# Kernel optimization log

Hardware: AMD Instinct MI355X
Metric: run time of the kernel (lower is better)

Reference implementation:

```python
import jax, jax.numpy as jnp
import numpy as np

L, V, C, H, T_MAX, FF = 8, 50257, 1024, 16, 1024, 4096
DH = C // H
EPS = 1e-5


def setup_inputs() -> dict:
    key = jax.random.key(0)
    ks = jax.random.split(key, 16)
    s = 0.02
    inp = {
        "idx": jax.random.randint(ks[0], (2, 1024), 0, V, dtype=jnp.int32),
        "tok_emb": jax.random.normal(ks[1], (V, C), jnp.float32) * s,
        "pos_emb": jax.random.normal(ks[2], (T_MAX, C), jnp.float32) * s,
        "qkv_w": jax.random.normal(ks[3], (L, C, 3 * C), jnp.float32) * s,
        "qkv_b": jnp.zeros((L, 3 * C), jnp.float32),
        "out_w": jax.random.normal(ks[4], (L, C, C), jnp.float32) * s,
        "out_b": jnp.zeros((L, C), jnp.float32),
        "ln1_s": jnp.ones((L, C), jnp.float32),
        "ln1_b": jnp.zeros((L, C), jnp.float32),
        "ln2_s": jnp.ones((L, C), jnp.float32),
        "ln2_b": jnp.zeros((L, C), jnp.float32),
        "ffn_w1": jax.random.normal(ks[5], (L, C, FF), jnp.float32) * s,
        "ffn_b1": jnp.zeros((L, FF), jnp.float32),
        "ffn_w2": jax.random.normal(ks[6], (L, FF, C), jnp.float32) * s,
        "ffn_b2": jnp.zeros((L, C), jnp.float32),
        "lnf_s": jnp.ones((C,), jnp.float32),
        "lnf_b": jnp.zeros((C,), jnp.float32),
    }
    return inp


def _layernorm(x, scale, bias):
    m = jnp.mean(x, axis=-1, keepdims=True)
    v = jnp.mean(jnp.square(x - m), axis=-1, keepdims=True)
    return (x - m) * jax.lax.rsqrt(v + EPS) * scale + bias


def reference(idx, tok_emb, pos_emb, qkv_w, qkv_b, out_w, out_b,
              ln1_s, ln1_b, ln2_s, ln2_b,
              ffn_w1, ffn_b1, ffn_w2, ffn_b2, lnf_s, lnf_b):
    B, T = idx.shape
    x = tok_emb[idx] + pos_emb[:T]          # [B,T,C]
    causal = jnp.tril(jnp.ones((T, T), bool))  # [T,T]
    scale = 1.0 / np.sqrt(DH)

    def block(x, p):
        qw, qb, ow, ob, l1s, l1b, l2s, l2b, w1, b1, w2, b2 = p
        h = _layernorm(x, l1s, l1b)
        qkv = h @ qw + qb                    # [B,T,3C]
        q, k, v = jnp.split(qkv, 3, axis=-1)
        q = q.reshape(B, T, H, DH).transpose(0, 2, 1, 3)  # [B,H,T,Dh]
        k = k.reshape(B, T, H, DH).transpose(0, 2, 1, 3)
        v = v.reshape(B, T, H, DH).transpose(0, 2, 1, 3)
        scores = jnp.einsum('bhqd,bhkd->bhqk', q, k) * scale
        scores = jnp.where(causal, scores, -jnp.inf)
        w = jax.nn.softmax(scores, axis=-1)
        o = jnp.einsum('bhqk,bhkd->bhqd', w, v)
        o = o.transpose(0, 2, 1, 3).reshape(B, T, C)
        x = x + (o @ ow + ob)
        h2 = _layernorm(x, l2s, l2b)
        x = x + (jax.nn.gelu(h2 @ w1 + b1, approximate=False) @ w2 + b2)
        return x, None

    params = (qkv_w, qkv_b, out_w, out_b, ln1_s, ln1_b, ln2_s, ln2_b,
              ffn_w1, ffn_b1, ffn_w2, ffn_b2)
    x, _ = jax.lax.scan(block, x, params)
    x = _layernorm(x, lnf_s, lnf_b)
    logits = x @ tok_emb.T                   # tied head, no bias
    return logits
```

## Files before the change

### kernel.cpp

```cpp
#include <hip/hip_runtime.h>
#include <hip/hip_bf16.h>

#define NL 8
#define NV 50257
#define NC 1024
#define NH 16
#define NT 1024
#define NFF 4096
#define NB 2
#define NM (NB*NT)

typedef __attribute__((ext_vector_type(8))) short bf16x8;
typedef __attribute__((ext_vector_type(4))) float f32x4;

__device__ __forceinline__ unsigned short f2bf(float f) {
    union { float f; unsigned u; } a; a.f = f;
    unsigned r = a.u + 0x7FFFu + ((a.u >> 16) & 1u);
    return (unsigned short)(r >> 16);
}

__device__ __forceinline__ void gload16(const unsigned short* g, unsigned short* l) {
    __builtin_amdgcn_global_load_lds(
        (const __attribute__((address_space(1))) unsigned int*)g,
        (__attribute__((address_space(3))) unsigned int*)l,
        16, 0, 0);
}

template<int VN> __device__ __forceinline__ void vwait() {
    asm volatile("s_waitcnt vmcnt(%0)" :: "n"(VN) : "memory");
}
__device__ __forceinline__ void barrier_mem() {
    asm volatile("" ::: "memory");
    __builtin_amdgcn_s_barrier();
    asm volatile("" ::: "memory");
}

__global__ __launch_bounds__(256) void embed_kernel(
    const int* __restrict__ idx, const float* __restrict__ te,
    const float* __restrict__ pe, float* __restrict__ x) {
    int row = blockIdx.x;
    int t = row & (NT - 1);
    int id = idx[row];
    const float4 a = reinterpret_cast<const float4*>(te + (size_t)id * NC)[threadIdx.x];
    const float4 b = reinterpret_cast<const float4*>(pe + (size_t)t * NC)[threadIdx.x];
    float4 o; o.x = a.x + b.x; o.y = a.y + b.y; o.z = a.z + b.z; o.w = a.w + b.w;
    reinterpret_cast<float4*>(x + (size_t)row * NC)[threadIdx.x] = o;
}

__global__ __launch_bounds__(256) void cvt_bf16_kernel(
    const float* __restrict__ in, unsigned short* __restrict__ out, size_t n4) {
    size_t i = (size_t)blockIdx.x * 256 + threadIdx.x;
    if (i >= n4) return;
    float4 v = reinterpret_cast<const float4*>(in)[i];
    uint2 u;
    u.x = (unsigned)f2bf(v.x) | ((unsigned)f2bf(v.y) << 16);
    u.y = (unsigned)f2bf(v.z) | ((unsigned)f2bf(v.w) << 16);
    reinterpret_cast<uint2*>(out)[i] = u;
}

__global__ __launch_bounds__(256) void wtrans4_kernel(
    const float* __restrict__ s0, const float* __restrict__ s1,
    const float* __restrict__ s2, const float* __restrict__ s3,
    unsigned short* __restrict__ d0, unsigned short* __restrict__ d1,
    unsigned short* __restrict__ d2, unsigned short* __restrict__ d3) {
    __shared__ float tile[32][33];
    int bid = blockIdx.x;
    const float* W; unsigned short* D; int K, N, tn, tk;
    if (bid < 3072)      { W = s0; D = d0; K = 1024; N = 3072; tn = bid % 96;  tk = bid / 96; }
    else if (bid < 4096) { int t = bid - 3072; W = s1; D = d1; K = 1024; N = 1024; tn = t & 31;  tk = t >> 5; }
    else if (bid < 8192) { int t = bid - 4096; W = s2; D = d2; K = 1024; N = 4096; tn = t & 127; tk = t >> 7; }
    else                 { int t = bid - 8192; W = s3; D = d3; K = 4096; N = 1024; tn = t & 31;  tk = t >> 5; }
    int n0 = tn * 32, k0 = tk * 32;
    int tx = threadIdx.x, ty = threadIdx.y;
#pragma unroll
    for (int i = 0; i < 4; ++i)
        tile[ty + i * 8][tx] = W[(size_t)(k0 + ty + i * 8) * N + n0 + tx];
    __syncthreads();
#pragma unroll
    for (int i = 0; i < 4; ++i)
        D[(size_t)(n0 + ty + i * 8) * K + k0 + tx] = f2bf(tile[tx][ty + i * 8]);
}

__global__ __launch_bounds__(256) void ln_kernel(
    const float* __restrict__ x, const float* __restrict__ gam,
    const float* __restrict__ bet, unsigned short* __restrict__ out) {
    __shared__ float red[4];
    int row = blockIdx.x, tid = threadIdx.x;
    const float4 v = reinterpret_cast<const float4*>(x + (size_t)row * NC)[tid];
    float s = v.x + v.y + v.z + v.w;
#pragma unroll
    for (int m = 32; m >= 1; m >>= 1) s += __shfl_xor(s, m, 64);
    if ((tid & 63) == 0) red[tid >> 6] = s;
    __syncthreads();
    float mean = (red[0] + red[1] + red[2] + red[3]) * (1.0f / NC);
    __syncthreads();
    float dx = v.x - mean, dy = v.y - mean, dz = v.z - mean, dw = v.w - mean;
    float q = dx * dx + dy * dy + dz * dz + dw * dw;
#pragma unroll
    for (int m = 32; m >= 1; m >>= 1) q += __shfl_xor(q, m, 64);
    if ((tid & 63) == 0) red[tid >> 6] = q;
    __syncthreads();
    float var = (red[0] + red[1] + red[2] + red[3]) * (1.0f / NC);
    float rstd = rsqrtf(var + 1e-5f);
    int c = tid * 4;
    const float4 g4 = reinterpret_cast<const float4*>(gam)[tid];
    const float4 b4 = reinterpret_cast<const float4*>(bet)[tid];
    uint2 u;
    u.x = (unsigned)f2bf(dx * rstd * g4.x + b4.x) |
          ((unsigned)f2bf(dy * rstd * g4.y + b4.y) << 16);
    u.y = (unsigned)f2bf(dz * rstd * g4.z + b4.z) |
          ((unsigned)f2bf(dw * rstd * g4.w + b4.w) << 16);
    reinterpret_cast<uint2*>(out + (size_t)row * NC + c)[0] = u;
}

template<int ACT, bool BIAS, bool OUTBF16, bool ATOMIC>
__global__ __launch_bounds__(256) void gemm_kernel(
    const unsigned short* __restrict__ A, const unsigned short* __restrict__ Bt,
    const float* __restrict__ bias, void* __restrict__ Cout,
    int N, int K, int ldc, int ksub) {
    __shared__ unsigned short As[2][128 * 32];
    __shared__ unsigned short Bs[2][128 * 32];
    const int tid = threadIdx.x;
    const int lane = tid & 63;
    const int wave = tid >> 6;
    const int wm = wave >> 1, wn = wave & 1;
    const int lr = lane & 15, lg = lane >> 4;
    const int m0 = blockIdx.x * 128, n0 = blockIdx.y * 128;
    const int kbeg = blockIdx.z * ksub, kend = kbeg + ksub;

    const int r0 = tid >> 2;
    const int c0 = (tid & 3) * 8;
    const unsigned short* Ag0 = A + (size_t)(m0 + r0) * K + c0;
    const unsigned short* Ag1 = A + (size_t)(m0 + r0 + 64) * K + c0;
    const unsigned short* Bg0 = Bt + (size_t)(n0 + r0) * K + c0;
    const unsigned short* Bg1 = Bt + (size_t)(n0 + r0 + 64) * K + c0;
    const int dw0 = wave * 512;
    const int dw1 = 2048 + wave * 512;

    const f32x4 zero4 = {0.0f, 0.0f, 0.0f, 0.0f};
    f32x4 acc[4][4];
#pragma unroll
    for (int i = 0; i < 4; ++i)
#pragma unroll
        for (int j = 0; j < 4; ++j) acc[i][j] = zero4;

    auto stage = [&](int buf, int k0) {
        gload16(Ag0 + k0, &As[buf][dw0]);
        gload16(Ag1 + k0, &As[buf][dw1]);
        gload16(Bg0 + k0, &Bs[buf][dw0]);
        gload16(Bg1 + k0, &Bs[buf][dw1]);
    };

    stage(0, kbeg);
    __syncthreads();
    int cur = 0;
    for (int k0 = kbeg; k0 < kend; k0 += 32) {
        if (k0 + 32 < kend) stage(cur ^ 1, k0 + 32);
        bf16x8 af[4], bfr[4];
#pragma unroll
        for (int f = 0; f < 4; ++f) {
            af[f]  = *reinterpret_cast<const bf16x8*>(&As[cur][(wm * 64 + f * 16 + lr) * 32 + lg * 8]);
            bfr[f] = *reinterpret_cast<const bf16x8*>(&Bs[cur][(wn * 64 + f * 16 + lr) * 32 + lg * 8]);
        }
#pragma unroll
        for (int i = 0; i < 4; ++i)
#pragma unroll
            for (int j = 0; j < 4; ++j)
                acc[i][j] = __builtin_amdgcn_mfma_f32_16x16x32_bf16(af[i], bfr[j], acc[i][j], 0, 0, 0);
        __syncthreads();
        cur ^= 1;
    }

#pragma unroll
    for (int i = 0; i < 4; ++i) {
#pragma unroll
        for (int j = 0; j < 4; ++j) {
            int col = n0 + wn * 64 + j * 16 + lr;
            float bv = (BIAS && kbeg == 0) ? bias[col] : 0.0f;
#pragma unroll
            for (int r = 0; r < 4; ++r) {
                int row = m0 + wm * 64 + i * 16 + lg * 4 + r;
                float v = acc[i][j][r] + bv;
                if (ACT == 1) v = 0.5f * v * (1.0f + erff(v * 0.70710678118654752f));
                if (ATOMIC) {
                    atomicAdd(reinterpret_cast<float*>(Cout) + (size_t)row * ldc + col, v);
                } else if (OUTBF16) {
                    reinterpret_cast<unsigned short*>(Cout)[(size_t)row * ldc + col] = f2bf(v);
                } else {
                    reinterpret_cast<float*>(Cout)[(size_t)row * ldc + col] = v;
                }
            }
        }
    }
}

__global__ __launch_bounds__(512, 2) void head_gemm_kernel(
    const unsigned short* __restrict__ A, const unsigned short* __restrict__ Bt,
    float* __restrict__ C, int N, int K) {
    __shared__ unsigned short lds[4][2][8192];
    const int tid = threadIdx.x;
    const int lane = tid & 63, wid = tid >> 6;
    const int wm = wid >> 2, wn = wid & 3;
    const int lr = lane & 15, lg = lane >> 4;

    const int qx = gridDim.x >> 3;
    const int orig = blockIdx.x;
    const int wg = (orig & 7) * qx + (orig >> 3);
    const int m0 = (wg & 7) * 256;
    const int n0 = (wg >> 3) * 256;

    const int o0 = tid, o1 = tid + 512;
    int rA0, kb0, rA1, kb1;
    { int pr = o0 >> 3, s = o0 & 7; int li = (s << 4) ^ ((pr & 7) << 4);
      rA0 = (pr << 1) | (li >> 6); kb0 = li & 63; }
    { int pr = o1 >> 3, s = o1 & 7; int li = (s << 4) ^ ((pr & 7) << 4);
      rA1 = (pr << 1) | (li >> 6); kb1 = li & 63; }
    const char* pA0 = (const char*)A + (size_t)(m0 + rA0) * (2 * K) + kb0;
    const char* pA1 = (const char*)A + (size_t)(m0 + rA1) * (2 * K) + kb1;
    const char* pB0 = (const char*)Bt + (size_t)min(n0 + rA0, N - 1) * (2 * K) + kb0;
    const char* pB1 = (const char*)Bt + (size_t)min(n0 + rA1, N - 1) * (2 * K) + kb1;
    const int dw0 = wid * 512;
    const int dw1 = 4096 + wid * 512;

    const int swz = (((lr & 1) << 6) | (lg << 4)) ^ (((lr >> 1) & 7) << 4);
    const int pbA = (wm * 64 + (lr >> 1)) * 128 + swz;
    const int pbB = (wn * 32 + (lr >> 1)) * 128 + swz;

    auto stage = [&](int slot, int koff) {
        unsigned short* la = &lds[slot][0][0];
        unsigned short* lb = &lds[slot][1][0];
        gload16((const unsigned short*)(pA0 + koff), la + dw0);
        gload16((const unsigned short*)(pA1 + koff), la + dw1);
        gload16((const unsigned short*)(pB0 + koff), lb + dw0);
        gload16((const unsigned short*)(pB1 + koff), lb + dw1);
    };
    auto rdA = [&](int slot, int mf) -> bf16x8 {
        return *reinterpret_cast<const bf16x8*>(
            (const char*)lds + slot * 32768 + pbA + mf * 1024);
    };
    auto rdB = [&](int slot, int nf) -> bf16x8 {
        return *reinterpret_cast<const bf16x8*>(
            (const char*)lds + slot * 32768 + 16384 + pbB + nf * 1024);
    };

    const f32x4 zero4 = {0.0f, 0.0f, 0.0f, 0.0f};
    f32x4 acc[8][4];
#pragma unroll
    for (int i = 0; i < 8; ++i)
#pragma unroll
        for (int j = 0; j < 4; ++j) acc[i][j] = zero4;

#define MFMA_ROW(AF, MI) \
    acc[MI][0] = __builtin_amdgcn_mfma_f32_16x16x32_bf16(AF, bf0, acc[MI][0], 0, 0, 0); \
    acc[MI][1] = __builtin_amdgcn_mfma_f32_16x16x32_bf16(AF, bf1, acc[MI][1], 0, 0, 0); \
    acc[MI][2] = __builtin_amdgcn_mfma_f32_16x16x32_bf16(AF, bf2, acc[MI][2], 0, 0, 0); \
    acc[MI][3] = __builtin_amdgcn_mfma_f32_16x16x32_bf16(AF, bf3, acc[MI][3], 0, 0, 0);

    stage(0, 0);
    stage(1, 64);
    const int nk = K >> 6;
    for (int t = 0; t < nk; ++t) {
        const int cur = (t & 1) << 1;
        const int koff = t << 7;
        const bool pf = (t + 1 < nk);
        vwait<4>();
        barrier_mem();
        if (pf) stage(cur ^ 2, koff + 128);
        bf16x8 bf0 = rdB(cur, 0), bf1 = rdB(cur, 1), bf2 = rdB(cur, 2), bf3 = rdB(cur, 3);
        bf16x8 a0 = rdA(cur, 0), a1 = rdA(cur, 1), a2 = rdA(cur, 2), a3 = rdA(cur, 3);
        __builtin_amdgcn_s_setprio(1);
        MFMA_ROW(a0, 0) MFMA_ROW(a1, 1) MFMA_ROW(a2, 2) MFMA_ROW(a3, 3)
        __builtin_amdgcn_s_setprio(0);
        if (pf) stage((cur ^ 2) | 1, koff + 192);
        a0 = rdA(cur, 4); a1 = rdA(cur, 5); a2 = rdA(cur, 6); a3 = rdA(cur, 7);
        __builtin_amdgcn_s_setprio(1);
        MFMA_ROW(a0, 4) MFMA_ROW(a1, 5) MFMA_ROW(a2, 6) MFMA_ROW(a3, 7)
        __builtin_amdgcn_s_setprio(0);
        if (pf) vwait<8>(); else vwait<0>();
        barrier_mem();
        const int nxt = cur | 1;
        bf0 = rdB(nxt, 0); bf1 = rdB(nxt, 1); bf2 = rdB(nxt, 2); bf3 = rdB(nxt, 3);
        a0 = rdA(nxt, 0); a1 = rdA(nxt, 1); a2 = rdA(nxt, 2); a3 = rdA(nxt, 3);
        __builtin_amdgcn_s_setprio(1);
        MFMA_ROW(a0, 0) MFMA_ROW(a1, 1) MFMA_ROW(a2, 2) MFMA_ROW(a3, 3)
        __builtin_amdgcn_s_setprio(0);
        a0 = rdA(nxt, 4); a1 = rdA(nxt, 5); a2 = rdA(nxt, 6); a3 = rdA(nxt, 7);
        __builtin_amdgcn_s_setprio(1);
        MFMA_ROW(a0, 4) MFMA_ROW(a1, 5) MFMA_ROW(a2, 6) MFMA_ROW(a3, 7)
        __builtin_amdgcn_s_setprio(0);
    }
#undef MFMA_ROW

#pragma unroll
    for (int mf = 0; mf < 8; ++mf)
#pragma unroll
        for (int nf = 0; nf < 4; ++nf) {
            int col = n0 + wn * 64 + nf * 16 + lr;
            if (col < N) {
#pragma unroll
                for (int r = 0; r < 4; ++r) {
                    int row = m0 + wm * 128 + mf * 16 + lg * 4 + r;
                    C[(size_t)row * N + col] = acc[mf][nf][r];
                }
            }
        }
}

__global__ __launch_bounds__(256) void vtrans_kernel(
    const unsigned short* __restrict__ qkv, unsigned short* __restrict__ vt) {
    __shared__ unsigned short tile[32][33];
    int bh = blockIdx.z; int b = bh >> 4, h = bh & 15;
    int t0 = blockIdx.x * 32, d0 = blockIdx.y * 32;
    int tx = threadIdx.x, ty = threadIdx.y;
#pragma unroll
    for (int i = 0; i < 4; ++i)
        tile[ty + i * 8][tx] =
            qkv[(size_t)(b * NT + t0 + ty + i * 8) * 3072 + 2048 + h * 64 + d0 + tx];
    __syncthreads();
#pragma unroll
    for (int i = 0; i < 4; ++i)
        vt[((size_t)(b * NH + h) * 64 + d0 + ty + i * 8) * NT + t0 + tx] = tile[tx][ty + i * 8];
}

__global__ __launch_bounds__(64) void attn_kernel(
    const unsigned short* __restrict__ qkv, const unsigned short* __restrict__ vt,
    unsigned short* __restrict__ o) {
    __shared__ unsigned short Vs[64][72];
    __shared__ unsigned short Ps[32][72];
    const int qt = blockIdx.x;
    const int h  = blockIdx.y;
    const int b  = blockIdx.z;
    const int lane = threadIdx.x;
    const int lr = lane & 15, lg = lane >> 4;

    const unsigned short* qbase = qkv + (size_t)(b * NT + qt * 32) * 3072 + h * 64;
    bf16x8 qf[2][2];
#pragma unroll
    for (int mf = 0; mf < 2; ++mf)
#pragma unroll
        for (int kc = 0; kc < 2; ++kc)
            qf[mf][kc] = *reinterpret_cast<const bf16x8*>(
                qbase + (size_t)(mf * 16 + lr) * 3072 + kc * 32 + lg * 8);

    const f32x4 zero4 = {0.0f, 0.0f, 0.0f, 0.0f};
    f32x4 oacc[2][4];
    float mrow[2][4], lsum[2][4];
#pragma unroll
    for (int mf = 0; mf < 2; ++mf) {
#pragma unroll
        for (int nf = 0; nf < 4; ++nf) oacc[mf][nf] = zero4;
#pragma unroll
        for (int r = 0; r < 4; ++r) { mrow[mf][r] = -INFINITY; lsum[mf][r] = 0.0f; }
    }

    const int qend = qt * 32 + 32;
    const int nkt = (qend + 63) >> 6;
    const unsigned short* kbase = qkv + (size_t)(b * NT) * 3072 + NC + h * 64;
    const unsigned short* vbase = vt + (size_t)((b * NH + h) * 64) * NT;

    for (int kt = 0; kt < nkt; ++kt) {
        __syncthreads();
#pragma unroll
        for (int i = 0; i < 8; ++i) {
            int chunk = lane + i * 64;
            int d = chunk >> 3;
            int kk = (chunk & 7) * 8;
            *reinterpret_cast<bf16x8*>(&Vs[d][kk]) =
                *reinterpret_cast<const bf16x8*>(vbase + (size_t)d * NT + kt * 64 + kk);
        }
        f32x4 s[2][4];
#pragma unroll
        for (int mf = 0; mf < 2; ++mf)
#pragma unroll
            for (int jf = 0; jf < 4; ++jf) s[mf][jf] = zero4;
#pragma unroll
        for (int kc = 0; kc < 2; ++kc) {
            bf16x8 kf[4];
#pragma unroll
            for (int jf = 0; jf < 4; ++jf)
                kf[jf] = *reinterpret_cast<const bf16x8*>(
                    kbase + (size_t)(kt * 64 + jf * 16 + lr) * 3072 + kc * 32 + lg * 8);
#pragma unroll
            for (int mf = 0; mf < 2; ++mf)
#pragma unroll
                for (int jf = 0; jf < 4; ++jf)
                    s[mf][jf] = __builtin_amdgcn_mfma_f32_16x16x32_bf16(
                        qf[mf][kc], kf[jf], s[mf][jf], 0, 0, 0);
        }
        const bool lastt = (kt == nkt - 1);
#pragma unroll
        for (int mf = 0; mf < 2; ++mf) {
#pragma unroll
            for (int r = 0; r < 4; ++r) {
                int rowg = qt * 32 + mf * 16 + lg * 4 + r;
                float tmax = -INFINITY;
#pragma unroll
                for (int jf = 0; jf < 4; ++jf) {
                    float v = s[mf][jf][r] * 0.125f;
                    if (lastt) {
                        int colg = kt * 64 + jf * 16 + lr;
                        if (colg > rowg) v = -INFINITY;
                    }
                    s[mf][jf][r] = v;
                    tmax = fmaxf(tmax, v);
                }
                tmax = fmaxf(tmax, __shfl_xor(tmax, 1, 64));
                tmax = fmaxf(tmax, __shfl_xor(tmax, 2, 64));
                tmax = fmaxf(tmax, __shfl_xor(tmax, 4, 64));
                tmax = fmaxf(tmax, __shfl_xor(tmax, 8, 64));
                float mnew = fmaxf(mrow[mf][r], tmax);
                float corr = __expf(mrow[mf][r] - mnew);
                float ps = 0.0f;
#pragma unroll
                for (int jf = 0; jf < 4; ++jf) {
                    float p = __expf(s[mf][jf][r] - mnew);
                    s[mf][jf][r] = p;
                    ps += p;
                }
                ps += __shfl_xor(ps, 1, 64);
                ps += __shfl_xor(ps, 2, 64);
                ps += __shfl_xor(ps, 4, 64);
                ps += __shfl_xor(ps, 8, 64);
                lsum[mf][r] = lsum[mf][r] * corr + ps;
                mrow[mf][r] = mnew;
#pragma unroll
                for (int nf = 0; nf < 4; ++nf) oacc[mf][nf][r] *= corr;
            }
        }
#pragma unroll
        for (int mf = 0; mf < 2; ++mf)
#pragma unroll
            for (int jf = 0; jf < 4; ++jf)
#pragma unroll
                for (int r = 0; r < 4; ++r)
                    Ps[mf * 16 + lg * 4 + r][jf * 16 + lr] = f2bf(s[mf][jf][r]);
        __syncthreads();
#pragma unroll
        for (int kc = 0; kc < 2; ++kc) {
            bf16x8 pf[2], vf[4];
#pragma unroll
            for (int mf = 0; mf < 2; ++mf)
                pf[mf] = *reinterpret_cast<const bf16x8*>(&Ps[mf * 16 + lr][kc * 32 + lg * 8]);
#pragma unroll
            for (int nf = 0; nf < 4; ++nf)
                vf[nf] = *reinterpret_cast<const bf16x8*>(&Vs[nf * 16 + lr][kc * 32 + lg * 8]);
#pragma unroll
            for (int mf = 0; mf < 2; ++mf)
#pragma unroll
                for (int nf = 0; nf < 4; ++nf)
                    oacc[mf][nf] = __builtin_amdgcn_mfma_f32_16x16x32_bf16(
                        pf[mf], vf[nf], oacc[mf][nf], 0, 0, 0);
        }
    }

    unsigned short* ob = o + (size_t)(b * NT + qt * 32) * NC + h * 64;
#pragma unroll
    for (int mf = 0; mf < 2; ++mf)
#pragma unroll
        for (int nf = 0; nf < 4; ++nf)
#pragma unroll
            for (int r = 0; r < 4; ++r) {
                float v = oacc[mf][nf][r] / lsum[mf][r];
                ob[(size_t)(mf * 16 + lg * 4 + r) * NC + nf * 16 + lr] = f2bf(v);
            }
}

extern "C" void kernel_launch(void* const* d_in, const int* in_sizes, int n_in,
                              void* d_out, int out_size, void* d_ws, size_t ws_size,
                              hipStream_t stream) {
    (void)in_sizes; (void)n_in; (void)out_size; (void)ws_size;
    const int*   idx    = (const int*)  d_in[0];
    const float* tok    = (const float*)d_in[1];
    const float* pos    = (const float*)d_in[2];
    const float* qkv_w  = (const float*)d_in[3];
    const float* qkv_b  = (const float*)d_in[4];
    const float* out_w  = (const float*)d_in[5];
    const float* out_b  = (const float*)d_in[6];
    const float* ln1_s  = (const float*)d_in[7];
    const float* ln1_b  = (const float*)d_in[8];
    const float* ln2_s  = (const float*)d_in[9];
    const float* ln2_b  = (const float*)d_in[10];
    const float* ffn_w1 = (const float*)d_in[11];
    const float* ffn_b1 = (const float*)d_in[12];
    const float* ffn_w2 = (const float*)d_in[13];
    const float* ffn_b2 = (const float*)d_in[14];
    const float* lnf_s  = (const float*)d_in[15];
    const float* lnf_b  = (const float*)d_in[16];

    char* p = (char*)d_ws;
    float* x              = (float*)p;          p += (size_t)NM * NC * 4;
    unsigned short* hbuf  = (unsigned short*)p; p += (size_t)NM * NC * 2;
    unsigned short* qkvb  = (unsigned short*)p; p += (size_t)NM * 3 * NC * 2;
    unsigned short* obuf  = (unsigned short*)p; p += (size_t)NM * NC * 2;
    unsigned short* gbuf  = (unsigned short*)p; p += (size_t)NM * NFF * 2;
    unsigned short* vtb   = (unsigned short*)p; p += (size_t)NB * NH * 64 * NT * 2;
    unsigned short* wq    = (unsigned short*)p; p += (size_t)3 * NC * NC * 2;
    unsigned short* wo    = (unsigned short*)p; p += (size_t)NC * NC * 2;
    unsigned short* w1    = (unsigned short*)p; p += (size_t)NC * NFF * 2;
    unsigned short* w2    = (unsigned short*)p; p += (size_t)NFF * NC * 2;
    unsigned short* temb  = (unsigned short*)p; p += (size_t)NV * NC * 2;

    {
        size_t n4 = (size_t)NV * NC / 4;
        int blocks = (int)((n4 + 255) / 256);
        cvt_bf16_kernel<<<blocks, 256, 0, stream>>>(tok, temb, n4);
    }
    embed_kernel<<<NM, 256, 0, stream>>>(idx, tok, pos, x);

    for (int l = 0; l < NL; ++l) {
        wtrans4_kernel<<<12288, dim3(32, 8), 0, stream>>>(
            qkv_w + (size_t)l * NC * 3 * NC, out_w + (size_t)l * NC * NC,
            ffn_w1 + (size_t)l * NC * NFF, ffn_w2 + (size_t)l * NFF * NC,
            wq, wo, w1, w2);

        ln_kernel<<<NM, 256, 0, stream>>>(x, ln1_s + (size_t)l * NC, ln1_b + (size_t)l * NC, hbuf);
        gemm_kernel<0, true, true, false><<<dim3(16, 24), 256, 0, stream>>>(
            hbuf, wq, qkv_b + (size_t)l * 3 * NC, qkvb, 3 * NC, NC, 3 * NC, NC);
        vtrans_kernel<<<dim3(32, 2, 32), dim3(32, 8), 0, stream>>>(qkvb, vtb);
        attn_kernel<<<dim3(32, 16, 2), 64, 0, stream>>>(qkvb, vtb, obuf);
        gemm_kernel<0, true, false, true><<<dim3(16, 8, 2), 256, 0, stream>>>(
            obuf, wo, out_b + (size_t)l * NC, x, NC, NC, NC, NC / 2);
        ln_kernel<<<NM, 256, 0, stream>>>(x, ln2_s + (size_t)l * NC, ln2_b + (size_t)l * NC, hbuf);
        gemm_kernel<1, true, true, false><<<dim3(16, 32), 256, 0, stream>>>(
            hbuf, w1, ffn_b1 + (size_t)l * NFF, gbuf, NFF, NC, NFF, NC);
        gemm_kernel<0, true, false, true><<<dim3(16, 8, 4), 256, 0, stream>>>(
            gbuf, w2, ffn_b2 + (size_t)l * NC, x, NC, NFF, NC, NFF / 4);
    }
    ln_kernel<<<NM, 256, 0, stream>>>(x, lnf_s, lnf_b, hbuf);
    head_gemm_kernel<<<dim3(8 * 197), 512, 0, stream>>>(hbuf, temb, (float*)d_out, NV, NC);
}
```

Measured before the change: 2.012 ms.

## Reschedule GEMM prefetch barriers and split attention query tile across two waves

The GEMM main loop now issues LDS fragment reads before starting the next global-to-LDS prefetch, and adds barriers and vmcnt waits at finer points so loads overlap the MFMA bursts more evenly. Separately, the attention kernel moves from one wave handling 32 query rows to two waves of 16 rows each, sharing the V tile staged in LDS. This halves per-wave register state and doubles waves per block to raise parallelism. The cost is that K fragments are now loaded once per wave, and each loop iteration carries extra barriers.

```diff
diff --git a/kernel.cpp b/kernel.cpp
--- a/kernel.cpp
+++ b/kernel.cpp
@@ -258,33 +258,36 @@
 
     stage(0, 0);
     stage(1, 64);
+    vwait<4>();
+    barrier_mem();
     const int nk = K >> 6;
     for (int t = 0; t < nk; ++t) {
         const int cur = (t & 1) << 1;
+        const int nxt = cur | 1;
         const int koff = t << 7;
         const bool pf = (t + 1 < nk);
-        vwait<4>();
-        barrier_mem();
-        if (pf) stage(cur ^ 2, koff + 128);
         bf16x8 bf0 = rdB(cur, 0), bf1 = rdB(cur, 1), bf2 = rdB(cur, 2), bf3 = rdB(cur, 3);
         bf16x8 a0 = rdA(cur, 0), a1 = rdA(cur, 1), a2 = rdA(cur, 2), a3 = rdA(cur, 3);
+        if (pf) stage(cur ^ 2, koff + 128);
+        barrier_mem();
         __builtin_amdgcn_s_setprio(1);
         MFMA_ROW(a0, 0) MFMA_ROW(a1, 1) MFMA_ROW(a2, 2) MFMA_ROW(a3, 3)
         __builtin_amdgcn_s_setprio(0);
-        if (pf) stage((cur ^ 2) | 1, koff + 192);
         a0 = rdA(cur, 4); a1 = rdA(cur, 5); a2 = rdA(cur, 6); a3 = rdA(cur, 7);
+        if (pf) { stage((cur ^ 2) | 1, koff + 192); vwait<8>(); } else { vwait<0>(); }
+        barrier_mem();
         __builtin_amdgcn_s_setprio(1);
         MFMA_ROW(a0, 4) MFMA_ROW(a1, 5) MFMA_ROW(a2, 6) MFMA_ROW(a3, 7)
         __builtin_amdgcn_s_setprio(0);
-        if (pf) vwait<8>(); else vwait<0>();
-        barrier_mem();
-        const int nxt = cur | 1;
         bf0 = rdB(nxt, 0); bf1 = rdB(nxt, 1); bf2 = rdB(nxt, 2); bf3 = rdB(nxt, 3);
         a0 = rdA(nxt, 0); a1 = rdA(nxt, 1); a2 = rdA(nxt, 2); a3 = rdA(nxt, 3);
+        barrier_mem();
         __builtin_amdgcn_s_setprio(1);
         MFMA_ROW(a0, 0) MFMA_ROW(a1, 1) MFMA_ROW(a2, 2) MFMA_ROW(a3, 3)
         __builtin_amdgcn_s_setprio(0);
         a0 = rdA(nxt, 4); a1 = rdA(nxt, 5); a2 = rdA(nxt, 6); a3 = rdA(nxt, 7);
+        if (pf) vwait<4>(); else vwait<0>();
+        barrier_mem();
         __builtin_amdgcn_s_setprio(1);
         MFMA_ROW(a0, 4) MFMA_ROW(a1, 5) MFMA_ROW(a2, 6) MFMA_ROW(a3, 7)
         __builtin_amdgcn_s_setprio(0);
@@ -322,7 +325,7 @@
         vt[((size_t)(b * NH + h) * 64 + d0 + ty + i * 8) * NT + t0 + tx] = tile[tx][ty + i * 8];
 }
 
-__global__ __launch_bounds__(64) void attn_kernel(
+__global__ __launch_bounds__(128) void attn_kernel(
     const unsigned short* __restrict__ qkv, const unsigned short* __restrict__ vt,
     unsigned short* __restrict__ o) {
     __shared__ unsigned short Vs[64][72];
@@ -330,28 +333,24 @@
     const int qt = blockIdx.x;
     const int h  = blockIdx.y;
     const int b  = blockIdx.z;
-    const int lane = threadIdx.x;
+    const int tid = threadIdx.x;
+    const int lane = tid & 63, wv = tid >> 6;
     const int lr = lane & 15, lg = lane >> 4;
 
-    const unsigned short* qbase = qkv + (size_t)(b * NT + qt * 32) * 3072 + h * 64;
-    bf16x8 qf[2][2];
-#pragma unroll
-    for (int mf = 0; mf < 2; ++mf)
-#pragma unroll
-        for (int kc = 0; kc < 2; ++kc)
-            qf[mf][kc] = *reinterpret_cast<const bf16x8*>(
-                qbase + (size_t)(mf * 16 + lr) * 3072 + kc * 32 + lg * 8);
+    const unsigned short* qbase = qkv + (size_t)(b * NT + qt * 32 + wv * 16) * 3072 + h * 64;
+    bf16x8 qf[2];
+#pragma unroll
+    for (int kc = 0; kc < 2; ++kc)
+        qf[kc] = *reinterpret_cast<const bf16x8*>(
+            qbase + (size_t)lr * 3072 + kc * 32 + lg * 8);
 
     const f32x4 zero4 = {0.0f, 0.0f, 0.0f, 0.0f};
-    f32x4 oacc[2][4];
-    float mrow[2][4], lsum[2][4];
-#pragma unroll
-    for (int mf = 0; mf < 2; ++mf) {
-#pragma unroll
-        for (int nf = 0; nf < 4; ++nf) oacc[mf][nf] = zero4;
-#pragma unroll
-        for (int r = 0; r < 4; ++r) { mrow[mf][r] = -INFINITY; lsum[mf][r] = 0.0f; }
-    }
+    f32x4 oacc[4];
+    float mrow[4], lsum[4];
+#pragma unroll
+    for (int nf = 0; nf < 4; ++nf) oacc[nf] = zero4;
+#pragma unroll
+    for (int r = 0; r < 4; ++r) { mrow[r] = -INFINITY; lsum[r] = 0.0f; }
 
     const int qend = qt * 32 + 32;
     const int nkt = (qend + 63) >> 6;
@@ -361,18 +360,16 @@
     for (int kt = 0; kt < nkt; ++kt) {
         __syncthreads();
 #pragma unroll
-        for (int i = 0; i < 8; ++i) {
-            int chunk = lane + i * 64;
+        for (int i = 0; i < 4; ++i) {
+            int chunk = tid + i * 128;
             int d = chunk >> 3;
             int kk = (chunk & 7) * 8;
             *reinterpret_cast<bf16x8*>(&Vs[d][kk]) =
                 *reinterpret_cast<const bf16x8*>(vbase + (size_t)d * NT + kt * 64 + kk);
         }
-        f32x4 s[2][4];
-#pragma unroll
-        for (int mf = 0; mf < 2; ++mf)
-#pragma unroll
-            for (int jf = 0; jf < 4; ++jf) s[mf][jf] = zero4;
+        f32x4 s[4];
+#pragma unroll
+        for (int jf = 0; jf < 4; ++jf) s[jf] = zero4;
 #pragma unroll
         for (int kc = 0; kc < 2; ++kc) {
             bf16x8 kf[4];
@@ -381,88 +378,75 @@
                 kf[jf] = *reinterpret_cast<const bf16x8*>(
                     kbase + (size_t)(kt * 64 + jf * 16 + lr) * 3072 + kc * 32 + lg * 8);
 #pragma unroll
-            for (int mf = 0; mf < 2; ++mf)
-#pragma unroll
-                for (int jf = 0; jf < 4; ++jf)
-                    s[mf][jf] = __builtin_amdgcn_mfma_f32_16x16x32_bf16(
-                        qf[mf][kc], kf[jf], s[mf][jf], 0, 0, 0);
+            for (int jf = 0; jf < 4; ++jf)
+                s[jf] = __builtin_amdgcn_mfma_f32_16x16x32_bf16(
+                    qf[kc], kf[jf], s[jf], 0, 0, 0);
         }
         const bool lastt = (kt == nkt - 1);
 #pragma unroll
-        for (int mf = 0; mf < 2; ++mf) {
-#pragma unroll
-            for (int r = 0; r < 4; ++r) {
-                int rowg = qt * 32 + mf * 16 + lg * 4 + r;
-                float tmax = -INFINITY;
-#pragma unroll
-                for (int jf = 0; jf < 4; ++jf) {
-                    float v = s[mf][jf][r] * 0.125f;
-                    if (lastt) {
-                        int colg = kt * 64 + jf * 16 + lr;
-                        if (colg > rowg) v = -INFINITY;
-                    }
-                    s[mf][jf][r] = v;
-                    tmax = fmaxf(tmax, v);
+        for (int r = 0; r < 4; ++r) {
+            int rowg = qt * 32 + wv * 16 + lg * 4 + r;
+            float tmax = -INFINITY;
+#pragma unroll
+            for (int jf = 0; jf < 4; ++jf) {
+                float v = s[jf][r] * 0.125f;
+                if (lastt) {
+                    int colg = kt * 64 + jf * 16 + lr;
+                    if (colg > rowg) v = -INFINITY;
                 }
-                tmax = fmaxf(tmax, __shfl_xor(tmax, 1, 64));
-                tmax = fmaxf(tmax, __shfl_xor(tmax, 2, 64));
-                tmax = fmaxf(tmax, __shfl_xor(tmax, 4, 64));
-                tmax = fmaxf(tmax, __shfl_xor(tmax, 8, 64));
-                float mnew = fmaxf(mrow[mf][r], tmax);
-                float corr = __expf(mrow[mf][r] - mnew);
-                float ps = 0.0f;
-#pragma unroll
-                for (int jf = 0; jf < 4; ++jf) {
-                    float p = __expf(s[mf][jf][r] - mnew);
-                    s[mf][jf][r] = p;
-                    ps += p;
-                }
-                ps += __shfl_xor(ps, 1, 64);
-                ps += __shfl_xor(ps, 2, 64);
-                ps += __shfl_xor(ps, 4, 64);
-                ps += __shfl_xor(ps, 8, 64);
-                lsum[mf][r] = lsum[mf][r] * corr + ps;
-                mrow[mf][r] = mnew;
-#pragma unroll
-                for (int nf = 0; nf < 4; ++nf) oacc[mf][nf][r] *= corr;
+                s[jf][r] = v;
+                tmax = fmaxf(tmax, v);
             }
-        }
-#pragma unroll
-        for (int mf = 0; mf < 2; ++mf)
-#pragma unroll
-            for (int jf = 0; jf < 4; ++jf)
-#pragma unroll
-                for (int r = 0; r < 4; ++r)
-                    Ps[mf * 16 + lg * 4 + r][jf * 16 + lr] = f2bf(s[mf][jf][r]);
+            tmax = fmaxf(tmax, __shfl_xor(tmax, 1, 64));
+            tmax = fmaxf(tmax, __shfl_xor(tmax, 2, 64));
+            tmax = fmaxf(tmax, __shfl_xor(tmax, 4, 64));
+            tmax = fmaxf(tmax, __shfl_xor(tmax, 8, 64));
+            float mnew = fmaxf(mrow[r], tmax);
+            float corr = __expf(mrow[r] - mnew);
+            float ps = 0.0f;
+#pragma unroll
+            for (int jf = 0; jf < 4; ++jf) {
+                float p = __expf(s[jf][r] - mnew);
+                s[jf][r] = p;
+                ps += p;
+            }
+            ps += __shfl_xor(ps, 1, 64);
+            ps += __shfl_xor(ps, 2, 64);
+            ps += __shfl_xor(ps, 4, 64);
+            ps += __shfl_xor(ps, 8, 64);
+            lsum[r] = lsum[r] * corr + ps;
+            mrow[r] = mnew;
+#pragma unroll
+            for (int nf = 0; nf < 4; ++nf) oacc[nf][r] *= corr;
+        }
+#pragma unroll
+        for (int jf = 0; jf < 4; ++jf)
+#pragma unroll
+            for (int r = 0; r < 4; ++r)
+                Ps[wv * 16 + lg * 4 + r][jf * 16 + lr] = f2bf(s[jf][r]);
         __syncthreads();
 #pragma unroll
         for (int kc = 0; kc < 2; ++kc) {
-            bf16x8 pf[2], vf[4];
-#pragma unroll
-            for (int mf = 0; mf < 2; ++mf)
-                pf[mf] = *reinterpret_cast<const bf16x8*>(&Ps[mf * 16 + lr][kc * 32 + lg * 8]);
+            bf16x8 pf, vf[4];
+            pf = *reinterpret_cast<const bf16x8*>(&Ps[wv * 16 + lr][kc * 32 + lg * 8]);
 #pragma unroll
             for (int nf = 0; nf < 4; ++nf)
                 vf[nf] = *reinterpret_cast<const bf16x8*>(&Vs[nf * 16 + lr][kc * 32 + lg * 8]);
 #pragma unroll
-            for (int mf = 0; mf < 2; ++mf)
-#pragma unroll
-                for (int nf = 0; nf < 4; ++nf)
-                    oacc[mf][nf] = __builtin_amdgcn_mfma_f32_16x16x32_bf16(
-                        pf[mf], vf[nf], oacc[mf][nf], 0, 0, 0);
+            for (int nf = 0; nf < 4; ++nf)
+                oacc[nf] = __builtin_amdgcn_mfma_f32_16x16x32_bf16(
+                    pf, vf[nf], oacc[nf], 0, 0, 0);
         }
     }
 
-    unsigned short* ob = o + (size_t)(b * NT + qt * 32) * NC + h * 64;
-#pragma unroll
-    for (int mf = 0; mf < 2; ++mf)
-#pragma unroll
-        for (int nf = 0; nf < 4; ++nf)
-#pragma unroll
-            for (int r = 0; r < 4; ++r) {
-                float v = oacc[mf][nf][r] / lsum[mf][r];
-                ob[(size_t)(mf * 16 + lg * 4 + r) * NC + nf * 16 + lr] = f2bf(v);
-            }
+    unsigned short* ob = o + (size_t)(b * NT + qt * 32 + wv * 16) * NC + h * 64;
+#pragma unroll
+    for (int nf = 0; nf < 4; ++nf)
+#pragma unroll
+        for (int r = 0; r < 4; ++r) {
+            float v = oacc[nf][r] / lsum[r];
+            ob[(size_t)(lg * 4 + r) * NC + nf * 16 + lr] = f2bf(v);
+        }
 }
 
 extern "C" void kernel_launch(void* const* d_in, const int* in_sizes, int n_in,
@@ -517,7 +501,7 @@
         gemm_kernel<0, true, true, false><<<dim3(16, 24), 256, 0, stream>>>(
             hbuf, wq, qkv_b + (size_t)l * 3 * NC, qkvb, 3 * NC, NC, 3 * NC, NC);
         vtrans_kernel<<<dim3(32, 2, 32), dim3(32, 8), 0, stream>>>(qkvb, vtb);
-        attn_kernel<<<dim3(32, 16, 2), 64, 0, stream>>>(qkvb, vtb, obuf);
+        attn_kernel<<<dim3(32, 16, 2), 128, 0, stream>>>(qkvb, vtb, obuf);
         gemm_kernel<0, true, false, true><<<dim3(16, 8, 2), 256, 0, stream>>>(
             obuf, wo, out_b + (size_t)l * NC, x, NC, NC, NC, NC / 2);
         ln_kernel<<<NM, 256, 0, stream>>>(x, ln2_s + (size_t)l * NC, ln2_b + (size_t)l * NC, hbuf);
```

Result: no change. 2.040 ms (+1.4%).

## Triple-buffer GEMM LDS tiles with two-deep async prefetch and vmcnt waits

Applied to the files above, without the earlier changes.

The GEMM main loop moves from a double-buffered LDS scheme with a full __syncthreads to a three-buffer ring that keeps two K-tiles in flight. Completion is tracked with partial vmcnt waits (vwait<4>/vwait<0>) plus a barrier, so later loads can stay outstanding while the current tile is computed. This is meant to hide global-load latency behind the MFMA work. In exchange it uses 50% more LDS, which may reduce occupancy. It also relies on the vwait and barrier_mem helpers defined elsewhere and assumes ksub is at least 64.

```diff
diff --git a/kernel.cpp b/kernel.cpp
--- a/kernel.cpp
+++ b/kernel.cpp
@@ -118,15 +118,14 @@
     const unsigned short* __restrict__ A, const unsigned short* __restrict__ Bt,
     const float* __restrict__ bias, void* __restrict__ Cout,
     int N, int K, int ldc, int ksub) {
-    __shared__ unsigned short As[2][128 * 32];
-    __shared__ unsigned short Bs[2][128 * 32];
+    __shared__ unsigned short lds[3][2][128 * 32];
     const int tid = threadIdx.x;
     const int lane = tid & 63;
     const int wave = tid >> 6;
     const int wm = wave >> 1, wn = wave & 1;
     const int lr = lane & 15, lg = lane >> 4;
     const int m0 = blockIdx.x * 128, n0 = blockIdx.y * 128;
-    const int kbeg = blockIdx.z * ksub, kend = kbeg + ksub;
+    const int kbeg = blockIdx.z * ksub;
 
     const int r0 = tid >> 2;
     const int c0 = (tid & 3) * 8;
@@ -145,30 +144,37 @@
         for (int j = 0; j < 4; ++j) acc[i][j] = zero4;
 
     auto stage = [&](int buf, int k0) {
-        gload16(Ag0 + k0, &As[buf][dw0]);
-        gload16(Ag1 + k0, &As[buf][dw1]);
-        gload16(Bg0 + k0, &Bs[buf][dw0]);
-        gload16(Bg1 + k0, &Bs[buf][dw1]);
+        gload16(Ag0 + k0, &lds[buf][0][dw0]);
+        gload16(Ag1 + k0, &lds[buf][0][dw1]);
+        gload16(Bg0 + k0, &lds[buf][1][dw0]);
+        gload16(Bg1 + k0, &lds[buf][1][dw1]);
     };
 
+    const int nt = ksub >> 5;
     stage(0, kbeg);
-    __syncthreads();
-    int cur = 0;
-    for (int k0 = kbeg; k0 < kend; k0 += 32) {
-        if (k0 + 32 < kend) stage(cur ^ 1, k0 + 32);
+    stage(1, kbeg + 32);
+    vwait<4>();
+    barrier_mem();
+    int b0 = 0, b1 = 1, b2 = 2;
+    for (int t = 0; t < nt; ++t) {
+        const bool pf = (t + 2 < nt);
+        if (pf) stage(b2, kbeg + (t + 2) * 32);
         bf16x8 af[4], bfr[4];
 #pragma unroll
         for (int f = 0; f < 4; ++f) {
-            af[f]  = *reinterpret_cast<const bf16x8*>(&As[cur][(wm * 64 + f * 16 + lr) * 32 + lg * 8]);
-            bfr[f] = *reinterpret_cast<const bf16x8*>(&Bs[cur][(wn * 64 + f * 16 + lr) * 32 + lg * 8]);
+            af[f]  = *reinterpret_cast<const bf16x8*>(&lds[b0][0][(wm * 64 + f * 16 + lr) * 32 + lg * 8]);
+            bfr[f] = *reinterpret_cast<const bf16x8*>(&lds[b0][1][(wn * 64 + f * 16 + lr) * 32 + lg * 8]);
         }
 #pragma unroll
         for (int i = 0; i < 4; ++i)
 #pragma unroll
             for (int j = 0; j < 4; ++j)
                 acc[i][j] = __builtin_amdgcn_mfma_f32_16x16x32_bf16(af[i], bfr[j], acc[i][j], 0, 0, 0);
-        __syncthreads();
-        cur ^= 1;
+        if (t + 1 < nt) {
+            if (pf) vwait<4>(); else vwait<0>();
+            barrier_mem();
+        }
+        int tmp = b0; b0 = b1; b1 = b2; b2 = tmp;
     }
 
 #pragma unroll
```

Measured after the change: 1.968 ms. 1.02x faster.
